# Kernel optimization log

Measured on AMD Instinct MI355X. Metric: run time of the kernel, lower is better.

## Reference

```python
import jax, jax.numpy as jnp
import numpy as np

OUT_FEATURES = 4096
IN_FEATURES = 4096
GROUP_SIZE = 128
NUMEL = OUT_FEATURES * IN_FEATURES  # 16777216


def setup_inputs() -> dict:
    key = jax.random.key(0)
    k1, k2, k3, k4, k5 = jax.random.split(key, 5)
    x = jax.random.normal(k1, (4, 2048, IN_FEATURES), dtype=jnp.float32)
    # two int4 values packed per byte -> NUMEL // 2 bytes
    packed = jax.random.randint(k2, (NUMEL // 2,), 0, 256, dtype=jnp.int32)
    # per-group scale/offset (NUMEL // GROUP_SIZE groups)
    scales = jax.random.uniform(k3, (NUMEL // GROUP_SIZE,), dtype=jnp.float32) * 0.1 + 1e-3
    offsets = jax.random.normal(k4, (NUMEL // GROUP_SIZE,), dtype=jnp.float32) * 0.01
    bias = jax.random.normal(k5, (OUT_FEATURES,), dtype=jnp.float32)
    return {"x": x, "packed": packed, "scales": scales, "offsets": offsets, "bias": bias}


def int4_dequantize(packed, scales, offsets):
    # low nibble, then high nibble, interleaved: [l0, h0, l1, h1, ...]
    low = packed & 15
    high = (packed >> 4) & 15
    q = jnp.stack([low, high], axis=1).reshape(-1).astype(jnp.float32)  # [NUMEL]
    groups = q.reshape(-1, GROUP_SIZE)  # [n_groups, group_size]
    w = groups * scales[:, None] + offsets[:, None]
    return w.reshape(OUT_FEATURES, IN_FEATURES)


def reference(x, packed, scales, offsets, bias):
    w = int4_dequantize(packed, scales, offsets)  # [out, in]
    # F.linear: y = x @ w.T + bias
    return jnp.einsum('bsi,oi->bso', x, w) + bias
```

## Files before the change

### kernel.cpp

```cpp
#include <hip/hip_runtime.h>
#include <stdint.h>

typedef __attribute__((ext_vector_type(4))) float  f32x4;
typedef __attribute__((ext_vector_type(4))) int    i32x4;
typedef __attribute__((ext_vector_type(8))) __bf16 bf16x8;

constexpr int M_DIM = 8192, N_DIM = 4096, K_DIM = 4096;

#define VMCNT(n) asm volatile("s_waitcnt vmcnt(" #n ")" ::: "memory")
#define LGKMCNT0 asm volatile("s_waitcnt lgkmcnt(0)" ::: "memory")
#define SB __builtin_amdgcn_sched_barrier(0)

__global__ __launch_bounds__(256) void cvt_x(const float* __restrict__ X,
                                             __bf16* __restrict__ Xb) {
  size_t i = ((size_t)blockIdx.x * 256 + threadIdx.x) * 8;
  const f32x4* src = (const f32x4*)(X + i);
  f32x4 a = src[0], b = src[1];
  bf16x8 v;
  v[0] = (__bf16)a[0]; v[1] = (__bf16)a[1]; v[2] = (__bf16)a[2]; v[3] = (__bf16)a[3];
  v[4] = (__bf16)b[0]; v[5] = (__bf16)b[1]; v[6] = (__bf16)b[2]; v[7] = (__bf16)b[3];
  *(bf16x8*)(Xb + i) = v;
}

__global__ __launch_bounds__(256) void deq_w(const int* __restrict__ P,
                                             const float* __restrict__ S,
                                             const float* __restrict__ O,
                                             __bf16* __restrict__ Wb) {
  size_t i = (size_t)blockIdx.x * 256 + threadIdx.x;
  const i32x4* src = (const i32x4*)(P + i * 16);
  int g = (int)(i >> 2);
  float s = S[g], o = O[g];
  __bf16* dst = Wb + i * 32;
#pragma unroll
  for (int j = 0; j < 4; ++j) {
    i32x4 p = src[j];
    bf16x8 v;
#pragma unroll
    for (int b = 0; b < 4; ++b) {
      int pv = p[b];
      v[2 * b]     = (__bf16)fmaf((float)(pv & 15), s, o);
      v[2 * b + 1] = (__bf16)fmaf((float)((pv >> 4) & 15), s, o);
    }
    *(bf16x8*)(dst + j * 8) = v;
  }
}

__device__ __forceinline__ void stage64(const char* g, size_t rs, char* l, int tid) {
  const int r = tid >> 3;
  const int c = ((tid & 7) * 16) ^ ((r & 7) << 4);
  __builtin_amdgcn_global_load_lds(
      (const __attribute__((address_space(1))) uint32_t*)(g + (size_t)r * rs + c),
      (__attribute__((address_space(3))) uint32_t*)(l + (tid >> 6) * 1024),
      16, 0, 0);
}

__device__ __forceinline__ void read_a(bf16x8 (&dst)[4], const char* Ab,
                                       int wm, int ln15, int lq, int mh, int ks) {
#pragma unroll
  for (int m4 = 0; m4 < 4; ++m4) {
    const int r = wm * 128 + (mh * 4 + m4) * 16 + ln15;
    const int sw = (r & 7) << 4;
    dst[m4] = *(const bf16x8*)(Ab + r * 128 + ((ks * 64 + lq * 16) ^ sw));
  }
}

__device__ __forceinline__ void read_b(bf16x8 (&dst)[4], const char* Bb,
                                       int wn, int ln15, int lq, int ks) {
#pragma unroll
  for (int n = 0; n < 4; ++n) {
    const int r = wn * 64 + n * 16 + ln15;
    const int sw = (r & 7) << 4;
    dst[n] = *(const bf16x8*)(Bb + r * 128 + ((ks * 64 + lq * 16) ^ sw));
  }
}

__device__ __forceinline__ void mfma16(f32x4 (&acc)[8][4], const bf16x8 (&af)[4],
                                       const bf16x8 (&bf)[4], int mbase) {
  __builtin_amdgcn_s_setprio(1);
#pragma unroll
  for (int m4 = 0; m4 < 4; ++m4)
#pragma unroll
    for (int n = 0; n < 4; ++n)
      acc[mbase + m4][n] = __builtin_amdgcn_mfma_f32_16x16x32_bf16(
          af[m4], bf[n], acc[mbase + m4][n], 0, 0, 0);
  __builtin_amdgcn_s_setprio(0);
}

__global__ __launch_bounds__(512, 2) void gemm8(const __bf16* __restrict__ A,
                                                const __bf16* __restrict__ B,
                                                const float* __restrict__ Bias,
                                                float* __restrict__ Y) {
  extern __shared__ char lds[];

  constexpr int NT = K_DIM / 64;
  const int tid  = threadIdx.x;
  const int lane = tid & 63;
  const int wid  = tid >> 6;
  const int wm   = wid >> 2;
  const int wn   = wid & 3;
  const int ln15 = lane & 15;
  const int lq   = lane >> 4;

  const int id  = blockIdx.y * gridDim.x + blockIdx.x;
  const int swz = (id & 7) * 64 + (id >> 3);
  const int bn0 = (swz & 15) * 256;
  const int bm0 = (swz >> 4) * 256;

  const size_t rs = (size_t)K_DIM * 2;
  const char* Ag = (const char*)A + (size_t)bm0 * rs;
  const char* Bg = (const char*)B + (size_t)bn0 * rs;

  f32x4 acc[8][4];
#pragma unroll
  for (int m = 0; m < 8; ++m)
#pragma unroll
    for (int n = 0; n < 4; ++n)
      acc[m][n] = (f32x4){0.f, 0.f, 0.f, 0.f};

  bf16x8 af0[4], af1[4], bf0[4], bf1[4];

  {
    char* Ab = lds;
    char* Bb = lds + 65536;
    stage64(Bg + (size_t)0 * rs,   rs, Bb + 0,     tid);
    stage64(Bg + (size_t)64 * rs,  rs, Bb + 8192,  tid);
    stage64(Bg + (size_t)128 * rs, rs, Bb + 16384, tid);
    stage64(Bg + (size_t)192 * rs, rs, Bb + 24576, tid);
    stage64(Ag + (size_t)0 * rs,   rs, Ab + 0,     tid);
    stage64(Ag + (size_t)128 * rs, rs, Ab + 16384, tid);
    stage64(Ag + (size_t)64 * rs,  rs, Ab + 8192,  tid);
    stage64(Ag + (size_t)192 * rs, rs, Ab + 24576, tid);
    char* Bn = lds + 65536 + 32768;
    stage64(Bg + 128,                 rs, Bn + 0,    tid);
    stage64(Bg + (size_t)64 * rs + 128, rs, Bn + 8192, tid);
  }
  VMCNT(4);
  SB;
  __builtin_amdgcn_s_barrier();
  read_b(bf0, lds + 65536, wn, ln15, lq, 0);
  read_a(af0, lds,         wm, ln15, lq, 0, 0);

  for (int t = 0; t < NT; ++t) {
    const char* Ab = lds + (t & 1) * 32768;
    const char* Bb = lds + 65536 + (t & 1) * 32768;
    char* An  = lds + ((t + 1) & 1) * 32768;
    char* Bn  = lds + 65536 + ((t + 1) & 1) * 32768;
    char* Bn2 = lds + 65536 + (t & 1) * 32768;
    const bool s1 = (t + 1 < NT);
    const bool s2 = (t + 2 < NT);
    const char* ga1 = Ag + (size_t)(t + 1) * 128;
    const char* gb1 = Bg + (size_t)(t + 1) * 128;
    const char* gb2 = Bg + (size_t)(t + 2) * 128;

    LGKMCNT0; SB;
    mfma16(acc, af0, bf0, 0);
    SB;
    if (s1) {
      stage64(gb1 + (size_t)128 * rs, rs, Bn + 16384, tid);
      stage64(gb1 + (size_t)192 * rs, rs, Bn + 24576, tid);
      stage64(ga1,                    rs, An + 0,     tid);
    }
    if (t == NT - 1) { VMCNT(0); } else { VMCNT(5); }
    SB;
    __builtin_amdgcn_s_barrier();
    read_a(af1, Ab, wm, ln15, lq, 1, 0);

    LGKMCNT0; SB;
    mfma16(acc, af1, bf0, 4);
    SB;
    if (s1) {
      stage64(ga1 + (size_t)128 * rs, rs, An + 16384, tid);
      stage64(ga1 + (size_t)64 * rs,  rs, An + 8192,  tid);
      stage64(ga1 + (size_t)192 * rs, rs, An + 24576, tid);
    }
    read_b(bf1, Bb, wn, ln15, lq, 1);
    read_a(af0, Ab, wm, ln15, lq, 0, 1);
    SB;
    __builtin_amdgcn_s_barrier();

    LGKMCNT0; SB;
    mfma16(acc, af0, bf1, 0);
    SB;
    read_a(af1, Ab, wm, ln15, lq, 1, 1);
    SB;
    __builtin_amdgcn_s_barrier();

    LGKMCNT0; SB;
    mfma16(acc, af1, bf1, 4);
    SB;
    if (s1) {
      VMCNT(2);
      SB;
      __builtin_amdgcn_s_barrier();
      if (s2) {
        stage64(gb2,                   rs, Bn2 + 0,    tid);
        stage64(gb2 + (size_t)64 * rs, rs, Bn2 + 8192, tid);
      }
      read_b(bf0, Bn, wn, ln15, lq, 0);
      read_a(af0, An, wm, ln15, lq, 0, 0);
    }
  }

#pragma unroll
  for (int n = 0; n < 4; ++n) {
    const int col = bn0 + wn * 64 + n * 16 + ln15;
    const float bias = Bias[col];
#pragma unroll
    for (int m = 0; m < 8; ++m) {
      const int row0 = bm0 + wm * 128 + m * 16 + lq * 4;
#pragma unroll
      for (int r = 0; r < 4; ++r)
        Y[(size_t)(row0 + r) * N_DIM + col] = acc[m][n][r] + bias;
    }
  }
}

__global__ __launch_bounds__(256) void qlin_fused_gemm(
    const float* __restrict__ X, const int* __restrict__ P,
    const float* __restrict__ S, const float* __restrict__ Ofs,
    const float* __restrict__ Bias, float* __restrict__ Y)
{
  constexpr int BM = 128, BN = 128, BK = 64;
  constexpr int NT = K_DIM / BK;
  __shared__ __bf16 As[BM * BK];
  __shared__ __bf16 Bs[BN * BK];

  const int tid  = threadIdx.x;
  const int lane = tid & 63;
  const int wv   = tid >> 6;
  const int wr   = (wv >> 1) * 64;
  const int wc   = (wv & 1) * 64;
  const int bn0 = blockIdx.x * BN;
  const int bm0 = blockIdx.y * BM;
  const int srow  = tid >> 1;
  const int shalf = tid & 1;

  const float* xrow = X + (size_t)(bm0 + srow) * K_DIM + shalf * 32;
  const int*   prow = P + (size_t)(bn0 + srow) * (K_DIM / 2) + shalf * 16;
  const int    gbase = (bn0 + srow) * (K_DIM / 128);

  const int rowb = srow * (BK * 2);
  const int sxor = (srow & 7) << 4;
  const int cbb  = shalf * 64;

  f32x4 areg[8];
  i32x4 breg[4];
  float sc, of;

  f32x4 acc[4][4];
#pragma unroll
  for (int i = 0; i < 4; ++i)
#pragma unroll
    for (int j = 0; j < 4; ++j)
      acc[i][j] = (f32x4){0.f, 0.f, 0.f, 0.f};

#pragma unroll
  for (int i = 0; i < 8; ++i) areg[i] = *(const f32x4*)(xrow + 4 * i);
#pragma unroll
  for (int i = 0; i < 4; ++i) breg[i] = *(const i32x4*)(prow + 4 * i);
  sc = S[gbase];
  of = Ofs[gbase];

  for (int kt = 0; kt < NT; ++kt) {
    __syncthreads();
    {
      char* ab = (char*)As + rowb;
      char* bb = (char*)Bs + rowb;
#pragma unroll
      for (int i = 0; i < 4; ++i) {
        bf16x8 v;
        f32x4 u0 = areg[2 * i], u1 = areg[2 * i + 1];
        v[0] = (__bf16)u0[0]; v[1] = (__bf16)u0[1];
        v[2] = (__bf16)u0[2]; v[3] = (__bf16)u0[3];
        v[4] = (__bf16)u1[0]; v[5] = (__bf16)u1[1];
        v[6] = (__bf16)u1[2]; v[7] = (__bf16)u1[3];
        *(bf16x8*)(ab + ((cbb + 16 * i) ^ sxor)) = v;
      }
#pragma unroll
      for (int i = 0; i < 4; ++i) {
        bf16x8 v;
        i32x4 p = breg[i];
#pragma unroll
        for (int j = 0; j < 4; ++j) {
          int pv = p[j];
          v[2 * j]     = (__bf16)fmaf((float)(pv & 15), sc, of);
          v[2 * j + 1] = (__bf16)fmaf((float)((pv >> 4) & 15), sc, of);
        }
        *(bf16x8*)(bb + ((cbb + 16 * i) ^ sxor)) = v;
      }
    }
    if (kt + 1 < NT) {
      const float* xp = xrow + (kt + 1) * BK;
#pragma unroll
      for (int i = 0; i < 8; ++i) areg[i] = *(const f32x4*)(xp + 4 * i);
      const int* pp = prow + (kt + 1) * (BK / 2);
#pragma unroll
      for (int i = 0; i < 4; ++i) breg[i] = *(const i32x4*)(pp + 4 * i);
      int g = gbase + (kt + 1) / 2;
      sc = S[g]; of = Ofs[g];
    }
    __syncthreads();
#pragma unroll
    for (int ks = 0; ks < 2; ++ks) {
      const int cb = ks * 64 + (lane >> 4) * 16;
      bf16x8 afr[4], bfr[4];
#pragma unroll
      for (int m = 0; m < 4; ++m) {
        int r = wr + m * 16 + (lane & 15);
        afr[m] = *(const bf16x8*)((const char*)As + r * (BK * 2) + (cb ^ ((r & 7) << 4)));
      }
#pragma unroll
      for (int n = 0; n < 4; ++n) {
        int r = wc + n * 16 + (lane & 15);
        bfr[n] = *(const bf16x8*)((const char*)Bs + r * (BK * 2) + (cb ^ ((r & 7) << 4)));
      }
#pragma unroll
      for (int m = 0; m < 4; ++m)
#pragma unroll
        for (int n = 0; n < 4; ++n)
          acc[m][n] = __builtin_amdgcn_mfma_f32_16x16x32_bf16(afr[m], bfr[n], acc[m][n], 0, 0, 0);
    }
  }
#pragma unroll
  for (int n = 0; n < 4; ++n) {
    const int col = bn0 + wc + n * 16 + (lane & 15);
    const float bias = Bias[col];
#pragma unroll
    for (int m = 0; m < 4; ++m) {
      const int row0 = bm0 + wr + m * 16 + (lane >> 4) * 4;
#pragma unroll
      for (int r = 0; r < 4; ++r)
        Y[(size_t)(row0 + r) * N_DIM + col] = acc[m][n][r] + bias;
    }
  }
}

extern "C" void kernel_launch(void* const* d_in, const int* in_sizes, int n_in,
                              void* d_out, int out_size, void* d_ws, size_t ws_size,
                              hipStream_t stream) {
  const float* X    = (const float*)d_in[0];
  const int*   P    = (const int*)d_in[1];
  const float* S    = (const float*)d_in[2];
  const float* Ofs  = (const float*)d_in[3];
  const float* Bias = (const float*)d_in[4];
  float* Y = (float*)d_out;

  const size_t xb_bytes = (size_t)M_DIM * K_DIM * 2;
  const size_t wb_bytes = (size_t)N_DIM * K_DIM * 2;

  if (ws_size >= xb_bytes + wb_bytes) {
    __bf16* Xb = (__bf16*)d_ws;
    __bf16* Wb = (__bf16*)((char*)d_ws + xb_bytes);

    cvt_x<<<dim3((M_DIM * K_DIM) / (256 * 8)), dim3(256), 0, stream>>>(X, Xb);
    deq_w<<<dim3((N_DIM * K_DIM) / (256 * 32)), dim3(256), 0, stream>>>(P, S, Ofs, Wb);

    hipFuncSetAttribute((const void*)gemm8,
                        hipFuncAttributeMaxDynamicSharedMemorySize, 131072);
    dim3 grid(N_DIM / 256, M_DIM / 256);
    gemm8<<<grid, dim3(512), 131072, stream>>>(Xb, Wb, Bias, Y);
  } else {
    dim3 grid(N_DIM / 128, M_DIM / 128);
    qlin_fused_gemm<<<grid, dim3(256), 0, stream>>>(X, P, S, Ofs, Bias, Y);
  }
}
```

Before: 268.4 us.

## Merge prep kernels and restructure GEMM wait/barrier placement

Combines the x-to-bf16 conversion and int4 weight dequantization into one launch, with blocks split by index, to save one kernel launch and its tail. In the GEMM main loop, the explicit lgkmcnt(0) waits are removed and the vmcnt wait plus barrier are moved to one point per iteration. LDS reads are now issued before the barriers so they can overlap with MFMA work. This leaves the compiler to insert LDS waits itself, and the changed vmcnt accounting risks reading LDS data that is not yet ready if the counts are wrong.

```diff
diff --git a/kernel.cpp b/kernel.cpp
--- a/kernel.cpp
+++ b/kernel.cpp
@@ -8,40 +8,44 @@
 constexpr int M_DIM = 8192, N_DIM = 4096, K_DIM = 4096;
 
 #define VMCNT(n) asm volatile("s_waitcnt vmcnt(" #n ")" ::: "memory")
-#define LGKMCNT0 asm volatile("s_waitcnt lgkmcnt(0)" ::: "memory")
 #define SB __builtin_amdgcn_sched_barrier(0)
 
-__global__ __launch_bounds__(256) void cvt_x(const float* __restrict__ X,
-                                             __bf16* __restrict__ Xb) {
-  size_t i = ((size_t)blockIdx.x * 256 + threadIdx.x) * 8;
-  const f32x4* src = (const f32x4*)(X + i);
-  f32x4 a = src[0], b = src[1];
-  bf16x8 v;
-  v[0] = (__bf16)a[0]; v[1] = (__bf16)a[1]; v[2] = (__bf16)a[2]; v[3] = (__bf16)a[3];
-  v[4] = (__bf16)b[0]; v[5] = (__bf16)b[1]; v[6] = (__bf16)b[2]; v[7] = (__bf16)b[3];
-  *(bf16x8*)(Xb + i) = v;
-}
-
-__global__ __launch_bounds__(256) void deq_w(const int* __restrict__ P,
-                                             const float* __restrict__ S,
-                                             const float* __restrict__ O,
-                                             __bf16* __restrict__ Wb) {
-  size_t i = (size_t)blockIdx.x * 256 + threadIdx.x;
-  const i32x4* src = (const i32x4*)(P + i * 16);
-  int g = (int)(i >> 2);
-  float s = S[g], o = O[g];
-  __bf16* dst = Wb + i * 32;
-#pragma unroll
-  for (int j = 0; j < 4; ++j) {
-    i32x4 p = src[j];
+constexpr int CVT_BLOCKS = (M_DIM * K_DIM) / (256 * 8);
+constexpr int DEQ_BLOCKS = (N_DIM * K_DIM) / (256 * 32);
+
+__global__ __launch_bounds__(256) void prep(const float* __restrict__ X,
+                                            const int* __restrict__ P,
+                                            const float* __restrict__ S,
+                                            const float* __restrict__ O,
+                                            __bf16* __restrict__ Xb,
+                                            __bf16* __restrict__ Wb) {
+  const int b = blockIdx.x;
+  if (b < CVT_BLOCKS) {
+    size_t i = ((size_t)b * 256 + threadIdx.x) * 8;
+    const f32x4* src = (const f32x4*)(X + i);
+    f32x4 a = src[0], c = src[1];
     bf16x8 v;
-#pragma unroll
-    for (int b = 0; b < 4; ++b) {
-      int pv = p[b];
-      v[2 * b]     = (__bf16)fmaf((float)(pv & 15), s, o);
-      v[2 * b + 1] = (__bf16)fmaf((float)((pv >> 4) & 15), s, o);
-    }
-    *(bf16x8*)(dst + j * 8) = v;
+    v[0] = (__bf16)a[0]; v[1] = (__bf16)a[1]; v[2] = (__bf16)a[2]; v[3] = (__bf16)a[3];
+    v[4] = (__bf16)c[0]; v[5] = (__bf16)c[1]; v[6] = (__bf16)c[2]; v[7] = (__bf16)c[3];
+    *(bf16x8*)(Xb + i) = v;
+  } else {
+    size_t i = (size_t)(b - CVT_BLOCKS) * 256 + threadIdx.x;
+    const i32x4* src = (const i32x4*)(P + i * 16);
+    int g = (int)(i >> 2);
+    float s = S[g], o = O[g];
+    __bf16* dst = Wb + i * 32;
+#pragma unroll
+    for (int j = 0; j < 4; ++j) {
+      i32x4 p = src[j];
+      bf16x8 v;
+#pragma unroll
+      for (int bb = 0; bb < 4; ++bb) {
+        int pv = p[bb];
+        v[2 * bb]     = (__bf16)fmaf((float)(pv & 15), s, o);
+        v[2 * bb + 1] = (__bf16)fmaf((float)((pv >> 4) & 15), s, o);
+      }
+      *(bf16x8*)(dst + j * 8) = v;
+    }
   }
 }
 
@@ -127,16 +131,16 @@
     stage64(Bg + (size_t)128 * rs, rs, Bb + 16384, tid);
     stage64(Bg + (size_t)192 * rs, rs, Bb + 24576, tid);
     stage64(Ag + (size_t)0 * rs,   rs, Ab + 0,     tid);
+    stage64(Ag + (size_t)64 * rs,  rs, Ab + 8192,  tid);
     stage64(Ag + (size_t)128 * rs, rs, Ab + 16384, tid);
-    stage64(Ag + (size_t)64 * rs,  rs, Ab + 8192,  tid);
     stage64(Ag + (size_t)192 * rs, rs, Ab + 24576, tid);
     char* Bn = lds + 65536 + 32768;
-    stage64(Bg + 128,                 rs, Bn + 0,    tid);
+    stage64(Bg + 128,                   rs, Bn + 0,    tid);
     stage64(Bg + (size_t)64 * rs + 128, rs, Bn + 8192, tid);
   }
-  VMCNT(4);
+  VMCNT(2);
+  __builtin_amdgcn_s_barrier();
   SB;
-  __builtin_amdgcn_s_barrier();
   read_b(bf0, lds + 65536, wn, ln15, lq, 0);
   read_a(af0, lds,         wm, ln15, lq, 0, 0);
 
@@ -152,22 +156,18 @@
     const char* gb1 = Bg + (size_t)(t + 1) * 128;
     const char* gb2 = Bg + (size_t)(t + 2) * 128;
 
-    LGKMCNT0; SB;
     mfma16(acc, af0, bf0, 0);
-    SB;
     if (s1) {
       stage64(gb1 + (size_t)128 * rs, rs, Bn + 16384, tid);
       stage64(gb1 + (size_t)192 * rs, rs, Bn + 24576, tid);
       stage64(ga1,                    rs, An + 0,     tid);
     }
-    if (t == NT - 1) { VMCNT(0); } else { VMCNT(5); }
+    read_a(af1, Ab, wm, ln15, lq, 1, 0);
     SB;
     __builtin_amdgcn_s_barrier();
-    read_a(af1, Ab, wm, ln15, lq, 1, 0);
-
-    LGKMCNT0; SB;
+    SB;
+
     mfma16(acc, af1, bf0, 4);
-    SB;
     if (s1) {
       stage64(ga1 + (size_t)128 * rs, rs, An + 16384, tid);
       stage64(ga1 + (size_t)64 * rs,  rs, An + 8192,  tid);
@@ -177,27 +177,28 @@
     read_a(af0, Ab, wm, ln15, lq, 0, 1);
     SB;
     __builtin_amdgcn_s_barrier();
-
-    LGKMCNT0; SB;
+    SB;
+
     mfma16(acc, af0, bf1, 0);
-    SB;
     read_a(af1, Ab, wm, ln15, lq, 1, 1);
     SB;
     __builtin_amdgcn_s_barrier();
-
-    LGKMCNT0; SB;
+    SB;
+
     mfma16(acc, af1, bf1, 4);
-    SB;
     if (s1) {
-      VMCNT(2);
-      SB;
-      __builtin_amdgcn_s_barrier();
       if (s2) {
         stage64(gb2,                   rs, Bn2 + 0,    tid);
         stage64(gb2 + (size_t)64 * rs, rs, Bn2 + 8192, tid);
-      }
+        VMCNT(2);
+      } else {
+        VMCNT(0);
+      }
+      __builtin_amdgcn_s_barrier();
+      SB;
       read_b(bf0, Bn, wn, ln15, lq, 0);
       read_a(af0, An, wm, ln15, lq, 0, 0);
+      SB;
     }
   }
 
@@ -352,8 +353,7 @@
     __bf16* Xb = (__bf16*)d_ws;
     __bf16* Wb = (__bf16*)((char*)d_ws + xb_bytes);
 
-    cvt_x<<<dim3((M_DIM * K_DIM) / (256 * 8)), dim3(256), 0, stream>>>(X, Xb);
-    deq_w<<<dim3((N_DIM * K_DIM) / (256 * 32)), dim3(256), 0, stream>>>(P, S, Ofs, Wb);
+    prep<<<dim3(CVT_BLOCKS + DEQ_BLOCKS), dim3(256), 0, stream>>>(X, P, S, Ofs, Xb, Wb);
 
     hipFuncSetAttribute((const void*)gemm8,
                         hipFuncAttributeMaxDynamicSharedMemorySize, 131072);
```

Result: no change. 264.9 us, median of 4 (-1.3%).
